# Kernel optimization log

Measured on AMD Instinct MI355X. Metric: run time of the kernel, lower is better.

## Reference

```python
import jax, jax.numpy as jnp
import numpy as np

WH, WW = 7, 7
NUM_HEADS = 12
DIM = 384
HEAD_DIM = DIM // NUM_HEADS
SCALE = HEAD_DIM ** -0.5


def _relative_position_index(Wh, Ww):
    coords = np.stack(np.meshgrid(np.arange(Wh), np.arange(Ww), indexing='ij'))  # (2, Wh, Ww)
    flat = coords.reshape(2, -1)  # (2, N)
    rel = flat[:, :, None] - flat[:, None, :]  # (2, N, N)
    rel = rel.transpose(1, 2, 0).astype(np.int64)  # (N, N, 2)
    rel[..., 0] += Wh - 1
    rel[..., 1] += Ww - 1
    rel[..., 0] *= 2 * Ww - 1
    return rel.sum(-1)  # (N, N)

REL_POS_INDEX = jnp.asarray(_relative_position_index(WH, WW))


def setup_inputs() -> dict:
    key = jax.random.key(0)
    ks = jax.random.split(key, 8)
    B_, N, C = 4096, WH * WW, DIM
    nW = 1024
    x = jax.random.normal(ks[0], (B_, N, C), dtype=jnp.float32)
    mask = jnp.zeros((nW, N, N), dtype=jnp.float32)
    qkv_w = jax.random.normal(ks[1], (3 * C, C), dtype=jnp.float32) * 0.02
    qkv_b = jnp.zeros((3 * C,), dtype=jnp.float32)
    proj_w = jax.random.normal(ks[2], (C, C), dtype=jnp.float32) * 0.02
    proj_b = jnp.zeros((C,), dtype=jnp.float32)
    rpb_table = jax.random.normal(ks[3], ((2 * WH - 1) * (2 * WW - 1), NUM_HEADS), dtype=jnp.float32) * 0.02
    lamb = jnp.zeros((NUM_HEADS,), dtype=jnp.float32)
    return {"x": x, "mask": mask, "qkv_w": qkv_w, "qkv_b": qkv_b,
            "proj_w": proj_w, "proj_b": proj_b, "rpb_table": rpb_table, "lamb": lamb}


def reference(x, mask, qkv_w, qkv_b, proj_w, proj_b, rpb_table, lamb):
    B_, N, C = x.shape
    H, hd = NUM_HEADS, HEAD_DIM
    # qkv projection: (B_, N, 3, H, hd)
    qkv = (x @ qkv_w.T + qkv_b).reshape(B_, N, 3, H, hd)
    q = qkv[:, :, 0].transpose(0, 2, 1, 3) * SCALE  # (B_, H, N, hd)
    k = qkv[:, :, 1].transpose(0, 2, 1, 3)
    v = qkv[:, :, 2].transpose(0, 2, 1, 3)
    attn = jnp.einsum('bhnd,bhmd->bhnm', q, k)  # (B_, H, N, N)
    # relative position bias gather: (N, N, H) -> (H, N, N)
    bias = rpb_table[REL_POS_INDEX.reshape(-1)].reshape(N, N, H).transpose(2, 0, 1)
    attn = attn + bias[None]
    nW = mask.shape[0]
    attn = attn.reshape(B_ // nW, nW, H, N, N) + mask[None, :, None]
    attn = attn.reshape(B_, H, N, N)
    attn = jax.nn.softmax(attn, axis=-1)
    # attn_scale rescale: attn_d is uniform 1/N
    attn_d = jnp.float32(1.0 / N)
    attn = attn_d + (attn - attn_d) * (1.0 + lamb)[None, :, None, None]
    out = jnp.einsum('bhnm,bhmd->bhnd', attn, v)  # (B_, H, N, hd)
    out = out.transpose(0, 2, 1, 3).reshape(B_, N, C)
    return out @ proj_w.T + proj_b
```

## Files before the change

kernel.cpp:

```cpp
#include <hip/hip_runtime.h>


#define SCALE_Q 0.17677669529663687f

typedef __bf16 bf16x8 __attribute__((ext_vector_type(8)));
typedef float f32x4 __attribute__((ext_vector_type(4)));

__device__ __forceinline__ unsigned short f2bf(float f) {
  union { float f; unsigned int u; } c; c.f = f;
  unsigned int u = c.u;
  return (unsigned short)((u + 0x7FFFu + ((u >> 16) & 1u)) >> 16);
}

__device__ __forceinline__ f32x4 mfma16(bf16x8 a, bf16x8 b, f32x4 c) {
  return __builtin_amdgcn_mfma_f32_16x16x32_bf16(a, b, c, 0, 0, 0);
}

__device__ __forceinline__ bf16x8 cvt8_frag(const float* __restrict__ src) {
  const float4 a = *(const float4*)src;
  const float4 b = *(const float4*)(src + 4);
  union { bf16x8 v; unsigned short u[8]; } c;
  c.u[0] = f2bf(a.x); c.u[1] = f2bf(a.y); c.u[2] = f2bf(a.z); c.u[3] = f2bf(a.w);
  c.u[4] = f2bf(b.x); c.u[5] = f2bf(b.y); c.u[6] = f2bf(b.z); c.u[7] = f2bf(b.w);
  return c.v;
}

__global__ void conv_w_kernel(const float* __restrict__ qkv_w,
                              const float* __restrict__ proj_w,
                              unsigned short* __restrict__ wbf) {
  const int f = blockIdx.x * 256 + threadIdx.x;
  const int lane = f & 63;
  const int l15 = lane & 15;
  const int quad = (lane >> 4) & 3;
  const float* src;
  unsigned short* dst;
  if (f < 55296) {
    const int rest = f >> 6;
    const int kk = rest % 12;
    const int ht = rest / 12;
    const int t = ht % 6, h = ht / 6;
    const int n96 = t * 16 + l15;
    const int grow = (n96 >> 5) * 384 + h * 32 + (n96 & 31);
    src = qkv_w + (size_t)grow * 384 + kk * 32 + quad * 8;
    dst = wbf + (size_t)f * 8;
  } else if (f < 73728) {
    const int p = f - 55296;
    const int rest = p >> 6;
    const int kk = rest % 12, t = rest / 12;
    src = proj_w + (size_t)(t * 16 + l15) * 384 + kk * 32 + quad * 8;
    dst = wbf + 442368 + (size_t)p * 8;
  } else {
    return;
  }
  const float4 a = *(const float4*)src;
  const float4 b = *(const float4*)(src + 4);
  ushort4 s0, s1;
  s0.x = f2bf(a.x); s0.y = f2bf(a.y); s0.z = f2bf(a.z); s0.w = f2bf(a.w);
  s1.x = f2bf(b.x); s1.y = f2bf(b.y); s1.z = f2bf(b.z); s1.w = f2bf(b.w);
  *(ushort4*)dst = s0;
  *(ushort4*)(dst + 4) = s1;
}

template <bool PRECONV>
__global__ __launch_bounds__(256, 2)
void attn_kernel(const float* __restrict__ x, const float* __restrict__ mask,
                 const float* __restrict__ qkv_w, const float* __restrict__ qkv_b,
                 const float* __restrict__ rpb, const float* __restrict__ lamb,
                 const unsigned short* __restrict__ qkv_w_bf,
                 float* __restrict__ out) {
  __shared__ __align__(16) unsigned short Xs[49][392];
  __shared__ __align__(16) unsigned short Qs[49][40];
  __shared__ __align__(16) unsigned short Ks[49][40];
  __shared__ __align__(16) unsigned short Vt[32][72];
  __shared__ __align__(16) float          Ss[49][52];
  __shared__ __align__(16) unsigned short Pb[49][72];
  __shared__ float Rpb[169 * 12];

  const int tid  = threadIdx.x;
  const int b    = blockIdx.x;
  const int lane = tid & 63;
  const int wv   = tid >> 6;
  const int l15  = lane & 15;
  const int quad = lane >> 4;

  {
    const float* xw = x + (size_t)b * (49 * 384);
    for (int t = tid; t < 49 * 96; t += 256) {
      int row = t / 96, c4 = t - row * 96;
      const float4 v = *(const float4*)(xw + row * 384 + c4 * 4);
      ushort4 s;
      s.x = f2bf(v.x); s.y = f2bf(v.y); s.z = f2bf(v.z); s.w = f2bf(v.w);
      *(ushort4*)&Xs[row][c4 * 4] = s;
    }
    for (int t = tid; t < 169 * 12; t += 256) Rpb[t] = rpb[t];
    for (int t = tid; t < 32 * 23; t += 256) {
      int d = t / 23, j = 49 + (t - d * 23);
      Vt[d][j] = 0;
    }
  }
  __syncthreads();

  const float* mbase = mask + (size_t)(b & 1023) * (49 * 49);

  for (int h = 0; h < 12; ++h) {
    {
      const int mp = wv >> 1, g = wv & 1;
      const int m0a = mp * 32;
      const int m0b = mp ? 33 : 16;
      const unsigned short* wg =
          qkv_w_bf + ((size_t)(h * 6 + g * 3) * 12) * 512 + lane * 8;
      f32x4 acc[2][3] = {};
      for (int kk = 0; kk < 12; ++kk) {
        const int k0 = kk * 32 + quad * 8;
        const bf16x8 a0 = *(const bf16x8*)&Xs[m0a + l15][k0];
        const bf16x8 a1 = *(const bf16x8*)&Xs[m0b + l15][k0];
#pragma unroll
        for (int e = 0; e < 3; ++e) {
          bf16x8 bb;
          if (PRECONV) {
            bb = *(const bf16x8*)(wg + (e * 12 + kk) * 512);
          } else {
            const int n96 = (g * 3 + e) * 16 + l15;
            const int grow = (n96 >> 5) * 384 + h * 32 + (n96 & 31);
            bb = cvt8_frag(qkv_w + (size_t)grow * 384 + k0);
          }
          acc[0][e] = mfma16(a0, bb, acc[0][e]);
          acc[1][e] = mfma16(a1, bb, acc[1][e]);
        }
      }
#pragma unroll
      for (int im = 0; im < 2; ++im) {
        const int m0 = im ? m0b : m0a;
#pragma unroll
        for (int e = 0; e < 3; ++e) {
          const int n96 = (g * 3 + e) * 16 + l15;
          const int sub = n96 >> 5, c32 = n96 & 31;
          const float bias = qkv_b[sub * 384 + h * 32 + c32];
#pragma unroll
          for (int r = 0; r < 4; ++r) {
            const int row = m0 + quad * 4 + r;
            const float val = acc[im][e][r] + bias;
            if (sub == 0)      Qs[row][c32] = f2bf(val * SCALE_Q);
            else if (sub == 1) Ks[row][c32] = f2bf(val);
            else               Vt[c32][row] = f2bf(val);
          }
        }
      }
    }
    __syncthreads();

    {
      const int m0 = (wv * 16 > 33) ? 33 : wv * 16;
      const bf16x8 aq = *(const bf16x8*)&Qs[m0 + l15][quad * 8];
      f32x4 sacc[4] = {};
#pragma unroll
      for (int nt = 0; nt < 4; ++nt) {
        const int n0 = (nt * 16 > 33) ? 33 : nt * 16;
        const bf16x8 bk = *(const bf16x8*)&Ks[n0 + l15][quad * 8];
        sacc[nt] = mfma16(aq, bk, sacc[nt]);
      }
#pragma unroll
      for (int nt = 0; nt < 4; ++nt) {
        const int n0 = (nt * 16 > 33) ? 33 : nt * 16;
#pragma unroll
        for (int r = 0; r < 4; ++r)
          Ss[m0 + quad * 4 + r][n0 + l15] = sacc[nt][r];
      }
    }
    __syncthreads();

    if (tid < 196) {
      const int i = tid >> 2, l4 = tid & 3;
      const int ri = (i * 37) >> 8;
      const int ci = i - ri * 7;
      const float* mrow = mbase + i * 49;
      float sv[13];
      float mx = -1e30f;
#pragma unroll
      for (int jj = 0; jj < 13; ++jj) {
        const int j = l4 + jj * 4;
        float val = -1e30f;
        if (j < 49) {
          const int rj = (j * 37) >> 8;
          const int cj = j - rj * 7;
          const int rel = (ri - rj + 6) * 13 + (ci - cj + 6);
          val = Ss[i][j] + Rpb[rel * 12 + h] + mrow[j];
        }
        sv[jj] = val;
        mx = fmaxf(mx, val);
      }
      mx = fmaxf(mx, __shfl_xor(mx, 1));
      mx = fmaxf(mx, __shfl_xor(mx, 2));
      float sum = 0.f;
#pragma unroll
      for (int jj = 0; jj < 13; ++jj) {
        const int j = l4 + jj * 4;
        const float e = (j < 49) ? __expf(sv[jj] - mx) : 0.f;
        sv[jj] = e;
        sum += e;
      }
      sum += __shfl_xor(sum, 1);
      sum += __shfl_xor(sum, 2);
      const float inv = 1.f / sum;
      const float lam = lamb[h];
      const float sc = 1.f + lam;
      const float ad = -lam * (1.0f / 49.0f);
#pragma unroll
      for (int jj = 0; jj < 16; ++jj) {
        const int j = l4 + jj * 4;
        float p = 0.f;
        if (j < 49) p = sv[jj] * inv * sc + ad;
        Pb[i][j] = f2bf(p);
      }
    }
    __syncthreads();

    {
      const int m0 = (wv * 16 > 33) ? 33 : wv * 16;
      f32x4 oacc[2] = {};
#pragma unroll
      for (int kk = 0; kk < 2; ++kk) {
        const int k0 = kk * 32 + quad * 8;
        const bf16x8 ap = *(const bf16x8*)&Pb[m0 + l15][k0];
#pragma unroll
        for (int nt = 0; nt < 2; ++nt) {
          const bf16x8 bv = *(const bf16x8*)&Vt[nt * 16 + l15][k0];
          oacc[nt] = mfma16(ap, bv, oacc[nt]);
        }
      }
#pragma unroll
      for (int nt = 0; nt < 2; ++nt)
#pragma unroll
        for (int r = 0; r < 4; ++r)
          Qs[m0 + quad * 4 + r][nt * 16 + l15] = f2bf(oacc[nt][r]);
    }
    __syncthreads();

    if (tid < 196) {
      const int row = tid >> 2, ch = tid & 3;
      const uint4 v = *(const uint4*)&Qs[row][ch * 8];
      *(uint4*)((char*)out + (size_t)(b * 49 + row) * 1536 + h * 64 + ch * 16) = v;
    }
    __syncthreads();
  }
}

template <bool PRECONV>
__global__ __launch_bounds__(256, 3)
void proj_kernel(const float* __restrict__ proj_w, const float* __restrict__ proj_b,
                 const unsigned short* __restrict__ proj_w_bf,
                 float* __restrict__ out) {
  __shared__ __align__(16) unsigned short Ains[64][392];
  const int tid  = threadIdx.x;
  const int mb   = blockIdx.x;
  const int lane = tid & 63;
  const int wv   = tid >> 6;
  const int l15  = lane & 15;
  const int quad = lane >> 4;

  for (int t = tid; t < 64 * 48; t += 256) {
    int row = t / 48, ch = t - row * 48;
    const uint4 v = *(const uint4*)((const char*)out +
        (size_t)(mb * 64 + row) * 1536 + ch * 16);
    *(uint4*)&Ains[row][ch * 8] = v;
  }
  __syncthreads();

  const int mp = wv >> 1, np = wv & 1;
  const unsigned short* pw = proj_w_bf + lane * 8;

  for (int nc = 0; nc < 6; ++nc) {
    const int t0 = nc * 4 + np * 2;
    f32x4 acc[2][2] = {};
    for (int kk = 0; kk < 12; ++kk) {
      const int k0 = kk * 32 + quad * 8;
      const bf16x8 a0 = *(const bf16x8*)&Ains[mp * 32 + l15][k0];
      const bf16x8 a1 = *(const bf16x8*)&Ains[mp * 32 + 16 + l15][k0];
      bf16x8 b0, b1;
      if (PRECONV) {
        b0 = *(const bf16x8*)(pw + (t0 * 12 + kk) * 512);
        b1 = *(const bf16x8*)(pw + ((t0 + 1) * 12 + kk) * 512);
      } else {
        b0 = cvt8_frag(proj_w + (size_t)(t0 * 16 + l15) * 384 + k0);
        b1 = cvt8_frag(proj_w + (size_t)((t0 + 1) * 16 + l15) * 384 + k0);
      }
      acc[0][0] = mfma16(a0, b0, acc[0][0]);
      acc[0][1] = mfma16(a0, b1, acc[0][1]);
      acc[1][0] = mfma16(a1, b0, acc[1][0]);
      acc[1][1] = mfma16(a1, b1, acc[1][1]);
    }
#pragma unroll
    for (int im = 0; im < 2; ++im) {
#pragma unroll
      for (int jn = 0; jn < 2; ++jn) {
        const int col = nc * 64 + np * 32 + jn * 16 + l15;
        const float pb = proj_b[col];
#pragma unroll
        for (int r = 0; r < 4; ++r) {
          const int token = mb * 64 + mp * 32 + im * 16 + quad * 4 + r;
          out[(size_t)token * 384 + col] = acc[im][jn][r] + pb;
        }
      }
    }
  }
}

extern "C" void kernel_launch(void* const* d_in, const int* in_sizes, int n_in,
                              void* d_out, int out_size, void* d_ws, size_t ws_size,
                              hipStream_t stream) {
  const float* x      = (const float*)d_in[0];
  const float* mask   = (const float*)d_in[1];
  const float* qkv_w  = (const float*)d_in[2];
  const float* qkv_b  = (const float*)d_in[3];
  const float* proj_w = (const float*)d_in[4];
  const float* proj_b = (const float*)d_in[5];
  const float* rpb    = (const float*)d_in[6];
  const float* lamb   = (const float*)d_in[7];
  float* out = (float*)d_out;

  const size_t conv_bytes = (size_t)(442368 + 147456) * sizeof(unsigned short);
  unsigned short* wbf = (unsigned short*)d_ws;

  if (ws_size >= conv_bytes) {
    conv_w_kernel<<<288, 256, 0, stream>>>(qkv_w, proj_w, wbf);
    attn_kernel<true><<<4096, 256, 0, stream>>>(x, mask, qkv_w, qkv_b, rpb, lamb,
                                                wbf, out);
    proj_kernel<true><<<3136, 256, 0, stream>>>(proj_w, proj_b, wbf + 442368, out);
  } else {
    attn_kernel<false><<<4096, 256, 0, stream>>>(x, mask, qkv_w, qkv_b, rpb, lamb,
                                                 nullptr, out);
    proj_kernel<false><<<3136, 256, 0, stream>>>(proj_w, proj_b, nullptr, out);
  }
}
```

Measured before the change: 1.353 ms.

## Restructure attention kernel: register softmax, k-major LDS layout, pregathered bias, smaller proj tiles

The attention kernel now keeps scores in MFMA accumulators and performs the softmax across lanes with shuffles. This removes the Ss shared buffer, a barrier and the separate softmax phase. Shared arrays are relaid out k-chunk-major to avoid padding and bank conflicts, and the per-window mask is loaded into registers once. The relative position bias is pre-gathered into a workspace table by the conversion kernel. The output is written directly via lane shuffles instead of staging through LDS, and occupancy targets are raised for both kernels, with the proj kernel using 32-row tiles. The cost is more register pressure and more blocks with less weight reuse in proj.

```diff
diff --git a/kernel.cpp b/kernel.cpp
--- a/kernel.cpp
+++ b/kernel.cpp
@@ -27,6 +27,7 @@
 
 __global__ void conv_w_kernel(const float* __restrict__ qkv_w,
                               const float* __restrict__ proj_w,
+                              const float* __restrict__ rpb,
                               unsigned short* __restrict__ wbf) {
   const int f = blockIdx.x * 256 + threadIdx.x;
   const int lane = f & 63;
@@ -49,6 +50,15 @@
     const int kk = rest % 12, t = rest / 12;
     src = proj_w + (size_t)(t * 16 + l15) * 384 + kk * 32 + quad * 8;
     dst = wbf + 442368 + (size_t)p * 8;
+  } else if (f < 73728 + 28812) {
+    const int t = f - 73728;
+    const int h = t / 2401, ij = t - h * 2401;
+    const int i = ij / 49, j = ij - (ij / 49) * 49;
+    const int ri = i / 7, ci = i - ri * 7;
+    const int rj = j / 7, cj = j - rj * 7;
+    const int rel = (ri - rj + 6) * 13 + (ci - cj + 6);
+    ((float*)(wbf + 589824))[t] = rpb[rel * 12 + h];
+    return;
   } else {
     return;
   }
@@ -62,19 +72,18 @@
 }
 
 template <bool PRECONV>
-__global__ __launch_bounds__(256, 2)
+__global__ __launch_bounds__(256, 3)
 void attn_kernel(const float* __restrict__ x, const float* __restrict__ mask,
                  const float* __restrict__ qkv_w, const float* __restrict__ qkv_b,
                  const float* __restrict__ rpb, const float* __restrict__ lamb,
                  const unsigned short* __restrict__ qkv_w_bf,
+                 const float* __restrict__ biasws,
                  float* __restrict__ out) {
-  __shared__ __align__(16) unsigned short Xs[49][392];
-  __shared__ __align__(16) unsigned short Qs[49][40];
-  __shared__ __align__(16) unsigned short Ks[49][40];
-  __shared__ __align__(16) unsigned short Vt[32][72];
-  __shared__ __align__(16) float          Ss[49][52];
-  __shared__ __align__(16) unsigned short Pb[49][72];
-  __shared__ float Rpb[169 * 12];
+  __shared__ __align__(16) unsigned short Xs[48][49][8];
+  __shared__ __align__(16) unsigned short Qs[4][49][8];
+  __shared__ __align__(16) unsigned short Ks[4][49][8];
+  __shared__ __align__(16) unsigned short Vt[8][32][8];
+  __shared__ __align__(16) unsigned short Pb[8][49][8];
 
   const int tid  = threadIdx.x;
   const int b    = blockIdx.x;
@@ -85,35 +94,48 @@
 
   {
     const float* xw = x + (size_t)b * (49 * 384);
-    for (int t = tid; t < 49 * 96; t += 256) {
-      int row = t / 96, c4 = t - row * 96;
-      const float4 v = *(const float4*)(xw + row * 384 + c4 * 4);
-      ushort4 s;
-      s.x = f2bf(v.x); s.y = f2bf(v.y); s.z = f2bf(v.z); s.w = f2bf(v.w);
-      *(ushort4*)&Xs[row][c4 * 4] = s;
-    }
-    for (int t = tid; t < 169 * 12; t += 256) Rpb[t] = rpb[t];
-    for (int t = tid; t < 32 * 23; t += 256) {
-      int d = t / 23, j = 49 + (t - d * 23);
-      Vt[d][j] = 0;
+    for (int t = tid; t < 49 * 48; t += 256) {
+      int row = t / 48, c = t - row * 48;
+      const float4 v0 = *(const float4*)(xw + row * 384 + c * 8);
+      const float4 v1 = *(const float4*)(xw + row * 384 + c * 8 + 4);
+      union { unsigned short u[8]; uint4 v; } s;
+      s.u[0] = f2bf(v0.x); s.u[1] = f2bf(v0.y); s.u[2] = f2bf(v0.z); s.u[3] = f2bf(v0.w);
+      s.u[4] = f2bf(v1.x); s.u[5] = f2bf(v1.y); s.u[6] = f2bf(v1.z); s.u[7] = f2bf(v1.w);
+      *(uint4*)&Xs[c][row][0] = s.v;
+    }
+    unsigned int* vz = (unsigned int*)&Vt[6][0][0];
+    if (tid < 256) vz[tid] = 0;
+    unsigned int* pz = (unsigned int*)&Pb[6][0][0];
+    for (int t = tid; t < 392; t += 256) pz[t] = 0;
+  }
+
+  const float* mbase = mask + (size_t)(b & 1023) * (49 * 49);
+
+  const int m0s = (wv * 16 > 33) ? 33 : wv * 16;
+
+  float mk[4][4];
+#pragma unroll
+  for (int r = 0; r < 4; ++r) {
+#pragma unroll
+    for (int nt = 0; nt < 4; ++nt) {
+      const int row = m0s + quad * 4 + r;
+      const int col = ((nt * 16 > 33) ? 33 : nt * 16) + l15;
+      mk[r][nt] = mbase[row * 49 + col];
     }
   }
   __syncthreads();
 
-  const float* mbase = mask + (size_t)(b & 1023) * (49 * 49);
-
   for (int h = 0; h < 12; ++h) {
+    const int mp = wv >> 1, g = wv & 1;
+    const int m0a = mp * 32;
+    const int m0b = mp ? 33 : 16;
+    f32x4 acc[2][3] = {};
     {
-      const int mp = wv >> 1, g = wv & 1;
-      const int m0a = mp * 32;
-      const int m0b = mp ? 33 : 16;
       const unsigned short* wg =
           qkv_w_bf + ((size_t)(h * 6 + g * 3) * 12) * 512 + lane * 8;
-      f32x4 acc[2][3] = {};
       for (int kk = 0; kk < 12; ++kk) {
-        const int k0 = kk * 32 + quad * 8;
-        const bf16x8 a0 = *(const bf16x8*)&Xs[m0a + l15][k0];
-        const bf16x8 a1 = *(const bf16x8*)&Xs[m0b + l15][k0];
+        const bf16x8 a0 = *(const bf16x8*)&Xs[kk * 4 + quad][m0a + l15][0];
+        const bf16x8 a1 = *(const bf16x8*)&Xs[kk * 4 + quad][m0b + l15][0];
 #pragma unroll
         for (int e = 0; e < 3; ++e) {
           bf16x8 bb;
@@ -122,135 +144,126 @@
           } else {
             const int n96 = (g * 3 + e) * 16 + l15;
             const int grow = (n96 >> 5) * 384 + h * 32 + (n96 & 31);
-            bb = cvt8_frag(qkv_w + (size_t)grow * 384 + k0);
+            bb = cvt8_frag(qkv_w + (size_t)grow * 384 + kk * 32 + quad * 8);
           }
           acc[0][e] = mfma16(a0, bb, acc[0][e]);
           acc[1][e] = mfma16(a1, bb, acc[1][e]);
         }
       }
-#pragma unroll
-      for (int im = 0; im < 2; ++im) {
-        const int m0 = im ? m0b : m0a;
-#pragma unroll
-        for (int e = 0; e < 3; ++e) {
-          const int n96 = (g * 3 + e) * 16 + l15;
-          const int sub = n96 >> 5, c32 = n96 & 31;
-          const float bias = qkv_b[sub * 384 + h * 32 + c32];
-#pragma unroll
-          for (int r = 0; r < 4; ++r) {
-            const int row = m0 + quad * 4 + r;
-            const float val = acc[im][e][r] + bias;
-            if (sub == 0)      Qs[row][c32] = f2bf(val * SCALE_Q);
-            else if (sub == 1) Ks[row][c32] = f2bf(val);
-            else               Vt[c32][row] = f2bf(val);
-          }
+    }
+    __syncthreads();
+
+#pragma unroll
+    for (int im = 0; im < 2; ++im) {
+      const int m0 = im ? m0b : m0a;
+#pragma unroll
+      for (int e = 0; e < 3; ++e) {
+        const int n96 = (g * 3 + e) * 16 + l15;
+        const int sub = n96 >> 5, c32 = n96 & 31;
+        const float bias = qkv_b[sub * 384 + h * 32 + c32];
+#pragma unroll
+        for (int r = 0; r < 4; ++r) {
+          const int row = m0 + quad * 4 + r;
+          const float val = acc[im][e][r] + bias;
+          if (sub == 0)      Qs[c32 >> 3][row][c32 & 7] = f2bf(val * SCALE_Q);
+          else if (sub == 1) Ks[c32 >> 3][row][c32 & 7] = f2bf(val);
+          else               Vt[row >> 3][c32][row & 7] = f2bf(val);
         }
       }
     }
     __syncthreads();
 
     {
-      const int m0 = (wv * 16 > 33) ? 33 : wv * 16;
-      const bf16x8 aq = *(const bf16x8*)&Qs[m0 + l15][quad * 8];
-      f32x4 sacc[4] = {};
+      const bf16x8 aq = *(const bf16x8*)&Qs[quad][m0s + l15][0];
+      f32x4 sacc[4];
 #pragma unroll
       for (int nt = 0; nt < 4; ++nt) {
         const int n0 = (nt * 16 > 33) ? 33 : nt * 16;
-        const bf16x8 bk = *(const bf16x8*)&Ks[n0 + l15][quad * 8];
-        sacc[nt] = mfma16(aq, bk, sacc[nt]);
-      }
-#pragma unroll
-      for (int nt = 0; nt < 4; ++nt) {
-        const int n0 = (nt * 16 > 33) ? 33 : nt * 16;
-#pragma unroll
-        for (int r = 0; r < 4; ++r)
-          Ss[m0 + quad * 4 + r][n0 + l15] = sacc[nt][r];
-      }
-    }
-    __syncthreads();
-
-    if (tid < 196) {
-      const int i = tid >> 2, l4 = tid & 3;
-      const int ri = (i * 37) >> 8;
-      const int ci = i - ri * 7;
-      const float* mrow = mbase + i * 49;
-      float sv[13];
-      float mx = -1e30f;
-#pragma unroll
-      for (int jj = 0; jj < 13; ++jj) {
-        const int j = l4 + jj * 4;
-        float val = -1e30f;
-        if (j < 49) {
-          const int rj = (j * 37) >> 8;
-          const int cj = j - rj * 7;
-          const int rel = (ri - rj + 6) * 13 + (ci - cj + 6);
-          val = Ss[i][j] + Rpb[rel * 12 + h] + mrow[j];
-        }
-        sv[jj] = val;
-        mx = fmaxf(mx, val);
-      }
-      mx = fmaxf(mx, __shfl_xor(mx, 1));
-      mx = fmaxf(mx, __shfl_xor(mx, 2));
-      float sum = 0.f;
-#pragma unroll
-      for (int jj = 0; jj < 13; ++jj) {
-        const int j = l4 + jj * 4;
-        const float e = (j < 49) ? __expf(sv[jj] - mx) : 0.f;
-        sv[jj] = e;
-        sum += e;
-      }
-      sum += __shfl_xor(sum, 1);
-      sum += __shfl_xor(sum, 2);
-      const float inv = 1.f / sum;
+        const bf16x8 bk = *(const bf16x8*)&Ks[quad][n0 + l15][0];
+        f32x4 z = {0.f, 0.f, 0.f, 0.f};
+        sacc[nt] = mfma16(aq, bk, z);
+      }
       const float lam = lamb[h];
       const float sc = 1.f + lam;
       const float ad = -lam * (1.0f / 49.0f);
-#pragma unroll
-      for (int jj = 0; jj < 16; ++jj) {
-        const int j = l4 + jj * 4;
-        float p = 0.f;
-        if (j < 49) p = sv[jj] * inv * sc + ad;
-        Pb[i][j] = f2bf(p);
+      const float* bh = biasws + h * 2401;
+#pragma unroll
+      for (int r = 0; r < 4; ++r) {
+        const int row = m0s + quad * 4 + r;
+        float val[4];
+#pragma unroll
+        for (int nt = 0; nt < 4; ++nt) {
+          const int col = ((nt * 16 > 33) ? 33 : nt * 16) + l15;
+          float bm;
+          if (PRECONV) {
+            bm = bh[row * 49 + col];
+          } else {
+            const int ri = (row * 37) >> 8, ci = row - ri * 7;
+            const int rj = (col * 37) >> 8, cj = col - rj * 7;
+            bm = rpb[((ri - rj + 6) * 13 + (ci - cj + 6)) * 12 + h];
+          }
+          val[nt] = sacc[nt][r] + bm + mk[r][nt];
+        }
+        float mx = fmaxf(fmaxf(val[0], val[1]), fmaxf(val[2], val[3]));
+        mx = fmaxf(mx, __shfl_xor(mx, 1));
+        mx = fmaxf(mx, __shfl_xor(mx, 2));
+        mx = fmaxf(mx, __shfl_xor(mx, 4));
+        mx = fmaxf(mx, __shfl_xor(mx, 8));
+        const float e0 = __expf(val[0] - mx);
+        const float e1 = __expf(val[1] - mx);
+        const float e2 = __expf(val[2] - mx);
+        const float e3 = __expf(val[3] - mx);
+        float s = e0 + e1 + e2 + ((l15 == 15) ? e3 : 0.f);
+        s += __shfl_xor(s, 1);
+        s += __shfl_xor(s, 2);
+        s += __shfl_xor(s, 4);
+        s += __shfl_xor(s, 8);
+        const float se = sc / s;
+        const int c0 = l15, c1 = 16 + l15, c2 = 32 + l15, c3 = 33 + l15;
+        Pb[c0 >> 3][row][c0 & 7] = f2bf(e0 * se + ad);
+        Pb[c1 >> 3][row][c1 & 7] = f2bf(e1 * se + ad);
+        Pb[c2 >> 3][row][c2 & 7] = f2bf(e2 * se + ad);
+        Pb[c3 >> 3][row][c3 & 7] = f2bf(e3 * se + ad);
       }
     }
     __syncthreads();
 
     {
-      const int m0 = (wv * 16 > 33) ? 33 : wv * 16;
       f32x4 oacc[2] = {};
 #pragma unroll
       for (int kk = 0; kk < 2; ++kk) {
-        const int k0 = kk * 32 + quad * 8;
-        const bf16x8 ap = *(const bf16x8*)&Pb[m0 + l15][k0];
+        const bf16x8 ap = *(const bf16x8*)&Pb[kk * 4 + quad][m0s + l15][0];
 #pragma unroll
         for (int nt = 0; nt < 2; ++nt) {
-          const bf16x8 bv = *(const bf16x8*)&Vt[nt * 16 + l15][k0];
+          const bf16x8 bv = *(const bf16x8*)&Vt[kk * 4 + quad][nt * 16 + l15][0];
           oacc[nt] = mfma16(ap, bv, oacc[nt]);
         }
       }
-#pragma unroll
-      for (int nt = 0; nt < 2; ++nt)
-#pragma unroll
-        for (int r = 0; r < 4; ++r)
-          Qs[m0 + quad * 4 + r][nt * 16 + l15] = f2bf(oacc[nt][r]);
-    }
-    __syncthreads();
-
-    if (tid < 196) {
-      const int row = tid >> 2, ch = tid & 3;
-      const uint4 v = *(const uint4*)&Qs[row][ch * 8];
-      *(uint4*)((char*)out + (size_t)(b * 49 + row) * 1536 + h * 64 + ch * 16) = v;
-    }
-    __syncthreads();
+      const int s0 = (quad << 4) | ((l15 & 7) << 1);
+#pragma unroll
+      for (int r = 0; r < 4; ++r) {
+        const float x00 = __shfl(oacc[0][r], s0);
+        const float x01 = __shfl(oacc[0][r], s0 + 1);
+        const float x10 = __shfl(oacc[1][r], s0);
+        const float x11 = __shfl(oacc[1][r], s0 + 1);
+        const float lo = (l15 < 8) ? x00 : x10;
+        const float hi = (l15 < 8) ? x01 : x11;
+        const unsigned int w =
+            ((unsigned int)f2bf(hi) << 16) | (unsigned int)f2bf(lo);
+        const int row = m0s + quad * 4 + r;
+        *(unsigned int*)((char*)out +
+            (size_t)(b * 49 + row) * 1536 + h * 64 + l15 * 4) = w;
+      }
+    }
   }
 }
 
 template <bool PRECONV>
-__global__ __launch_bounds__(256, 3)
+__global__ __launch_bounds__(256, 6)
 void proj_kernel(const float* __restrict__ proj_w, const float* __restrict__ proj_b,
                  const unsigned short* __restrict__ proj_w_bf,
                  float* __restrict__ out) {
-  __shared__ __align__(16) unsigned short Ains[64][392];
+  __shared__ __align__(16) unsigned short Ains[32][392];
   const int tid  = threadIdx.x;
   const int mb   = blockIdx.x;
   const int lane = tid & 63;
@@ -258,10 +271,10 @@
   const int l15  = lane & 15;
   const int quad = lane >> 4;
 
-  for (int t = tid; t < 64 * 48; t += 256) {
+  for (int t = tid; t < 32 * 48; t += 256) {
     int row = t / 48, ch = t - row * 48;
     const uint4 v = *(const uint4*)((const char*)out +
-        (size_t)(mb * 64 + row) * 1536 + ch * 16);
+        (size_t)(mb * 32 + row) * 1536 + ch * 16);
     *(uint4*)&Ains[row][ch * 8] = v;
   }
   __syncthreads();
@@ -271,35 +284,29 @@
 
   for (int nc = 0; nc < 6; ++nc) {
     const int t0 = nc * 4 + np * 2;
-    f32x4 acc[2][2] = {};
+    f32x4 acc[2] = {};
     for (int kk = 0; kk < 12; ++kk) {
       const int k0 = kk * 32 + quad * 8;
-      const bf16x8 a0 = *(const bf16x8*)&Ains[mp * 32 + l15][k0];
-      const bf16x8 a1 = *(const bf16x8*)&Ains[mp * 32 + 16 + l15][k0];
+      const bf16x8 a = *(const bf16x8*)&Ains[mp * 16 + l15][k0];
       bf16x8 b0, b1;
       if (PRECONV) {
-        b0 = *(const bf16x8*)(pw + (t0 * 12 + kk) * 512);
-        b1 = *(const bf16x8*)(pw + ((t0 + 1) * 12 + kk) * 512);
+        b0 = *(const bf16x8*)(pw + (size_t)(t0 * 12 + kk) * 512);
+        b1 = *(const bf16x8*)(pw + (size_t)((t0 + 1) * 12 + kk) * 512);
       } else {
         b0 = cvt8_frag(proj_w + (size_t)(t0 * 16 + l15) * 384 + k0);
         b1 = cvt8_frag(proj_w + (size_t)((t0 + 1) * 16 + l15) * 384 + k0);
       }
-      acc[0][0] = mfma16(a0, b0, acc[0][0]);
-      acc[0][1] = mfma16(a0, b1, acc[0][1]);
-      acc[1][0] = mfma16(a1, b0, acc[1][0]);
-      acc[1][1] = mfma16(a1, b1, acc[1][1]);
-    }
-#pragma unroll
-    for (int im = 0; im < 2; ++im) {
-#pragma unroll
-      for (int jn = 0; jn < 2; ++jn) {
-        const int col = nc * 64 + np * 32 + jn * 16 + l15;
-        const float pb = proj_b[col];
-#pragma unroll
-        for (int r = 0; r < 4; ++r) {
-          const int token = mb * 64 + mp * 32 + im * 16 + quad * 4 + r;
-          out[(size_t)token * 384 + col] = acc[im][jn][r] + pb;
-        }
+      acc[0] = mfma16(a, b0, acc[0]);
+      acc[1] = mfma16(a, b1, acc[1]);
+    }
+#pragma unroll
+    for (int jn = 0; jn < 2; ++jn) {
+      const int col = nc * 64 + np * 32 + jn * 16 + l15;
+      const float pb = proj_b[col];
+#pragma unroll
+      for (int r = 0; r < 4; ++r) {
+        const int token = mb * 32 + mp * 16 + quad * 4 + r;
+        out[(size_t)token * 384 + col] = acc[jn][r] + pb;
       }
     }
   }
@@ -318,17 +325,18 @@
   const float* lamb   = (const float*)d_in[7];
   float* out = (float*)d_out;
 
-  const size_t conv_bytes = (size_t)(442368 + 147456) * sizeof(unsigned short);
+  const size_t conv_bytes = (size_t)589824 * 2 + (size_t)28812 * 4;
   unsigned short* wbf = (unsigned short*)d_ws;
+  const float* biasws = (const float*)(wbf + 589824);
 
   if (ws_size >= conv_bytes) {
-    conv_w_kernel<<<288, 256, 0, stream>>>(qkv_w, proj_w, wbf);
+    conv_w_kernel<<<401, 256, 0, stream>>>(qkv_w, proj_w, rpb, wbf);
     attn_kernel<true><<<4096, 256, 0, stream>>>(x, mask, qkv_w, qkv_b, rpb, lamb,
-                                                wbf, out);
-    proj_kernel<true><<<3136, 256, 0, stream>>>(proj_w, proj_b, wbf + 442368, out);
+                                                wbf, biasws, out);
+    proj_kernel<true><<<6272, 256, 0, stream>>>(proj_w, proj_b, wbf + 442368, out);
   } else {
     attn_kernel<false><<<4096, 256, 0, stream>>>(x, mask, qkv_w, qkv_b, rpb, lamb,
-                                                 nullptr, out);
-    proj_kernel<false><<<3136, 256, 0, stream>>>(proj_w, proj_b, nullptr, out);
-  }
-}
+                                                 nullptr, nullptr, out);
+    proj_kernel<false><<<6272, 256, 0, stream>>>(proj_w, proj_b, nullptr, out);
+  }
+}
```

New measurement: 1.690 ms. 24.9% more time.
